# Optimization experiments

Hardware: AMD Instinct MI355X
Metric: run time of the kernel (lower is better)

The kernel has to match this reference:

```python
import jax, jax.numpy as jnp
import numpy as np

EPS = 1e-05
H, N, F = 1024, 16, 4096  # hidden_dim, state_dim, ffn_dim


def layernorm(x, g, b):
    mu = jnp.mean(x, axis=-1, keepdims=True)
    var = jnp.mean(jnp.square(x - mu), axis=-1, keepdims=True)
    return (x - mu) * jax.lax.rsqrt(var + EPS) * g + b


def setup_inputs() -> dict:
    key = jax.random.key(0)
    ks = jax.random.split(key, 12)
    B, L = 2, 2048
    s = lambda fan_in: 1.0 / np.sqrt(fan_in)
    inp = {
        "x": jax.random.normal(ks[0], (B, L, H), jnp.float32),
        "ln1_g": jnp.ones((H,), jnp.float32),
        "ln1_b": jnp.zeros((H,), jnp.float32),
        "Wd": jax.random.uniform(ks[1], (H, H), jnp.float32, -s(H), s(H)),
        "bd": jnp.zeros((H,), jnp.float32),
        "Wbc": jax.random.uniform(ks[2], (2 * N, H), jnp.float32, -s(H), s(H)),
        "bbc": jnp.zeros((2 * N,), jnp.float32),
        "A_log": jnp.log(jnp.tile(jnp.arange(1, N + 1, dtype=jnp.float32), (H, 1))),
        "D": jnp.ones((H,), jnp.float32),
        "ln2_g": jnp.ones((H,), jnp.float32),
        "ln2_b": jnp.zeros((H,), jnp.float32),
        "W1": jax.random.uniform(ks[3], (F, H), jnp.float32, -s(H), s(H)),
        "b1": jnp.zeros((F,), jnp.float32),
        "W2": jax.random.uniform(ks[4], (H, F), jnp.float32, -s(F), s(F)),
        "b2": jnp.zeros((H,), jnp.float32),
    }
    return inp


def _selective_ssm(xn, delta, Bm, Cm, A, D):
    # xn: (B,L,H)  delta: (B,L,H)  Bm,Cm: (B,L,N)  A: (H,N)  D: (H,)
    Bsz = xn.shape[0]
    # time-major for scan
    xs = (jnp.moveaxis(delta, 1, 0), jnp.moveaxis(Bm, 1, 0),
          jnp.moveaxis(Cm, 1, 0), jnp.moveaxis(xn, 1, 0))

    def step(h, t):
        d_t, b_t, c_t, x_t = t  # (B,H), (B,N), (B,N), (B,H)
        dA = jnp.exp(d_t[:, :, None] * A)                      # (B,H,N)
        dBx = d_t[:, :, None] * b_t[:, None, :] * x_t[:, :, None]
        h = dA * h + dBx                                       # (B,H,N)
        y = jnp.einsum('bhn,bn->bh', h, c_t)                   # (B,H)
        return h, y

    h0 = jnp.zeros((Bsz, H, N), xn.dtype)
    _, ys = jax.lax.scan(step, h0, xs)
    y = jnp.moveaxis(ys, 0, 1)  # (B,L,H)
    return y + D * xn


def reference(x, ln1_g, ln1_b, Wd, bd, Wbc, bbc, A_log, D,
              ln2_g, ln2_b, W1, b1, W2, b2):
    # --- SSMLayer: pre-norm selective SSM + residual ---
    xn = layernorm(x, ln1_g, ln1_b)
    delta = jax.nn.softplus(xn @ Wd.T + bd)      # (B,L,H)
    bc = xn @ Wbc.T + bbc                        # (B,L,2N)
    Bm, Cm = bc[..., :N], bc[..., N:]
    A = -jnp.exp(A_log)                          # (H,N), negative real
    ssm_out = x + _selective_ssm(xn, delta, Bm, Cm, A, D)
    # --- MambaBlock: norm -> FFN -> residual with ssm_out ---
    normed = layernorm(ssm_out, ln2_g, ln2_b)
    hff = jax.nn.gelu(normed @ W1.T + b1, approximate=False)
    ffn_out = hff @ W2.T + b2
    return ffn_out + ssm_out
```

## Files before the change

### kernel.cpp

```cpp
#include <hip/hip_runtime.h>
#include <cstdint>
#include <cstddef>

typedef unsigned short USHORT;
typedef __bf16 bf16x8 __attribute__((ext_vector_type(8)));
typedef float f32x4 __attribute__((ext_vector_type(4)));

__device__ __forceinline__ float b2f(USHORT u) {
    union { unsigned int i; float f; } v; v.i = ((unsigned int)u) << 16; return v.f;
}
__device__ __forceinline__ USHORT f2bf(float f) {
    union { float f; unsigned int i; } v; v.f = f;
    unsigned int u = v.i;
    unsigned int r = (u + 0x7FFFu + ((u >> 16) & 1u)) >> 16;
    return (USHORT)r;
}
__device__ __forceinline__ float fexp2(float x) { return __builtin_amdgcn_exp2f(x); }

__device__ __forceinline__ void gload_lds16(const void* g, void* l) {
    __builtin_amdgcn_global_load_lds(
        (const __attribute__((address_space(1))) void*)(uintptr_t)g,
        (__attribute__((address_space(3))) void*)(uint32_t)(uintptr_t)l,
        16, 0, 0);
}

__global__ __launch_bounds__(256)
void f2b_kernel(const float* __restrict__ src, USHORT* __restrict__ dst, int n)
{
    int i = (blockIdx.x * 256 + threadIdx.x) * 4;
    if (i < n) {
        float4 v = *(const float4*)(src + i);
        ushort4 o;
        o.x = f2bf(v.x); o.y = f2bf(v.y); o.z = f2bf(v.z); o.w = f2bf(v.w);
        *(ushort4*)(dst + i) = o;
    }
}

__global__ __launch_bounds__(256)
void ln_kernel(const float* __restrict__ inp, const float* __restrict__ g,
               const float* __restrict__ bsh, USHORT* __restrict__ out)
{
    const int tid = threadIdx.x;
    const size_t row = blockIdx.x;
    float4 t = ((const float4*)inp)[row * 256 + tid];
    float v[4] = { t.x, t.y, t.z, t.w };
    float s = v[0] + v[1] + v[2] + v[3];
    float sq = v[0]*v[0] + v[1]*v[1] + v[2]*v[2] + v[3]*v[3];
    #pragma unroll
    for (int off = 32; off; off >>= 1) { s += __shfl_down(s, off); sq += __shfl_down(sq, off); }
    __shared__ float red[8];
    const int wv = tid >> 6;
    if ((tid & 63) == 0) { red[wv] = s; red[wv + 4] = sq; }
    __syncthreads();
    const float S  = red[0] + red[1] + red[2] + red[3];
    const float SQ = red[4] + red[5] + red[6] + red[7];
    const float mu = S * (1.0f / 1024.0f);
    const float var = SQ * (1.0f / 1024.0f) - mu * mu;
    const float rs = rsqrtf(var + 1e-5f);
    float4 gv = ((const float4*)g)[tid];
    float4 bv = ((const float4*)bsh)[tid];
    ushort4 o;
    o.x = f2bf((v[0] - mu) * rs * gv.x + bv.x);
    o.y = f2bf((v[1] - mu) * rs * gv.y + bv.y);
    o.z = f2bf((v[2] - mu) * rs * gv.z + bv.z);
    o.w = f2bf((v[3] - mu) * rs * gv.w + bv.w);
    ((ushort4*)out)[row * 256 + tid] = o;
}

template<int EPI>
__global__ __launch_bounds__(256)
void gemm_bt(const USHORT* __restrict__ A, const USHORT* __restrict__ B,
             const float* __restrict__ bias, void* __restrict__ outp,
             void* __restrict__ outp2, int M, int N, int K, int lda, int ldb)
{
    __shared__ __align__(16) unsigned char smem[32768];
    USHORT* As = (USHORT*)smem;
    USHORT* Bs = (USHORT*)(smem + 8192);
    const int tid = threadIdx.x;
    const int lane = tid & 63;
    const int w = tid >> 6;
    const int wr = w >> 1, wc = w & 1;

    const int nx = gridDim.x, ny = gridDim.y;
    const int pid = blockIdx.y * nx + blockIdx.x;
    const int npg = 8 * nx;
    const int gid = pid / npg;
    const int first = gid * 8;
    const int rem = ny - first;
    const int gsz = (rem < 8) ? rem : 8;
    const int py = first + (pid % npg) % gsz;
    const int px = (pid % npg) / gsz;
    const int tm = py * 128;
    const int tn = px * 128;

    f32x4 acc[4][4];
    #pragma unroll
    for (int i = 0; i < 4; i++)
        #pragma unroll
        for (int j = 0; j < 4; j++) acc[i][j] = (f32x4){0.f, 0.f, 0.f, 0.f};

    const int srow = tid >> 2;
    const int scol = (tid & 3) * 8;
    const USHORT* gA0 = A + (size_t)(tm + srow) * lda + scol;
    const USHORT* gA1 = A + (size_t)(tm + 64 + srow) * lda + scol;
    const USHORT* gB0 = B + (size_t)(tn + srow) * ldb + scol;
    const USHORT* gB1 = B + (size_t)(tn + 64 + srow) * ldb + scol;
    USHORT* lA0 = As + w * 512;
    USHORT* lA1 = As + 2048 + w * 512;
    USHORT* lB0 = Bs + w * 512;
    USHORT* lB1 = Bs + 2048 + w * 512;

    const int fr = lane & 15;
    const int fko = (lane >> 4) * 8;
    const int quad = lane >> 4;

    for (int k0 = 0; k0 < K; k0 += 64) {
        gload_lds16(gA0 + k0, lA0);
        gload_lds16(gA1 + k0, lA1);
        gload_lds16(gB0 + k0, lB0);
        gload_lds16(gB1 + k0, lB1);
        gload_lds16(gA0 + k0 + 32, lA0 + 8192);
        gload_lds16(gA1 + k0 + 32, lA1 + 8192);
        gload_lds16(gB0 + k0 + 32, lB0 + 8192);
        gload_lds16(gB1 + k0 + 32, lB1 + 8192);
        __syncthreads();
        #pragma unroll
        for (int h = 0; h < 2; h++) {
            const USHORT* Ah = As + h * 8192;
            const USHORT* Bh = Bs + h * 8192;
            bf16x8 af[4], bfr[4];
            #pragma unroll
            for (int i = 0; i < 4; i++) {
                af[i]  = *(const bf16x8*)(Ah + (wr * 64 + i * 16 + fr) * 32 + fko);
                bfr[i] = *(const bf16x8*)(Bh + (wc * 64 + i * 16 + fr) * 32 + fko);
            }
            #pragma unroll
            for (int i = 0; i < 4; i++)
                #pragma unroll
                for (int j = 0; j < 4; j++)
                    acc[i][j] = __builtin_amdgcn_mfma_f32_16x16x32_bf16(af[i], bfr[j], acc[i][j], 0, 0, 0);
        }
        __syncthreads();
    }

    float* eW = (float*)(smem + (size_t)w * 4352);
    const int rr = lane >> 5;
    const int cc = lane & 31;
    const int gcolb = tn + wc * 64;
    float2 bvv = *(const float2*)&bias[gcolb + cc * 2];

    #pragma unroll
    for (int i = 0; i < 4; i++) {
        #pragma unroll
        for (int j = 0; j < 4; j++)
            #pragma unroll
            for (int r = 0; r < 4; r++)
                eW[(quad * 4 + r) * 68 + j * 16 + fr] = acc[i][j][r];
        __syncthreads();
        const int grow0 = tm + wr * 64 + i * 16;
        #pragma unroll
        for (int rp = 0; rp < 8; rp++) {
            const int row = rp * 2 + rr;
            const float2 v = *(const float2*)&eW[row * 68 + cc * 2];
            const size_t gidx = (size_t)(grow0 + row) * N + gcolb + cc * 2;
            if constexpr (EPI == 2) {
                const float z0 = v.x + bvv.x, z1 = v.y + bvv.y;
                const float o0 = (z0 > 20.f) ? z0 : 0.69314718f * __log2f(1.f + fexp2(z0 * 1.44269504f));
                const float o1 = (z1 > 20.f) ? z1 : 0.69314718f * __log2f(1.f + fexp2(z1 * 1.44269504f));
                *(float2*)((float*)outp + gidx) = make_float2(o0, o1);
            }
        }
        __syncthreads();
    }
    (void)outp2; (void)M;
}

template<int EPI>
__global__ __launch_bounds__(512)
void gemm256(const USHORT* __restrict__ A, const USHORT* __restrict__ B,
             const float* __restrict__ bias, void* __restrict__ outp,
             void* __restrict__ outp2, int M, int N, int K, int lda, int ldb)
{
    __shared__ __align__(16) unsigned char smem[131072];
    const int tid = threadIdx.x;
    const int lane = tid & 63;
    const int w = tid >> 6;
    const int wr = w >> 2;
    const int wc = w & 3;

    const int gx = gridDim.x;
    const int pid = blockIdx.y * gx + blockIdx.x;
    const int nwg = gx * gridDim.y;
    const int cpx = nwg >> 3;
    const int s = (pid & 7) * cpx + (pid >> 3);
    const int px = s % gx;
    const int py = s / gx;
    const int tm = py * 256;
    const int tn = px * 256;

    USHORT* po = nullptr;
    if constexpr (EPI == 3) {
        const int z = blockIdx.z;
        A += (size_t)z * K;
        B += (size_t)z * K;
        po = ((z < 2) ? (USHORT*)outp : (USHORT*)outp2) + (size_t)(z & 1) * ((size_t)M * N);
    }

    const int sr = tid >> 2;
    const int su = (tid & 3) ^ ((tid >> 3) & 3);
    const USHORT* gA0 = A + (size_t)(tm + sr) * lda + su * 8;
    const USHORT* gA1 = A + (size_t)(tm + 128 + sr) * lda + su * 8;
    const USHORT* gB0 = B + (size_t)(tn + sr) * ldb + su * 8;
    const USHORT* gB1 = B + (size_t)(tn + 128 + sr) * ldb + su * 8;

    const int fr = lane & 15;
    const int quad = lane >> 4;
    const int uR = quad ^ ((fr >> 1) & 3);
    const int loff = fr * 32 + uR * 8;

    f32x4 acc[8][4];
    #pragma unroll
    for (int i = 0; i < 8; i++)
        #pragma unroll
        for (int j = 0; j < 4; j++) acc[i][j] = (f32x4){0.f, 0.f, 0.f, 0.f};

    const int NT = K >> 5;

    auto stage = [&](int t) {
        unsigned char* sb = smem + (size_t)(t & 3) * 32768;
        const size_t koff = (size_t)t * 32;
        gload_lds16(gA0 + koff, sb + w * 1024);
        gload_lds16(gA1 + koff, sb + 8192 + w * 1024);
        gload_lds16(gB0 + koff, sb + 16384 + w * 1024);
        gload_lds16(gB1 + koff, sb + 24576 + w * 1024);
    };

    stage(0);
    stage(1);

    for (int t = 0; t < NT; ++t) {
        if (t + 1 < NT) asm volatile("s_waitcnt vmcnt(4)" ::: "memory");
        else            asm volatile("s_waitcnt vmcnt(0)" ::: "memory");
        __builtin_amdgcn_s_barrier();
        if (t + 2 < NT) stage(t + 2);

        const USHORT* sA = (const USHORT*)(smem + (size_t)(t & 3) * 32768);
        const USHORT* sB = sA + 8192;
        bf16x8 a[4], b[4];
        #pragma unroll
        for (int j = 0; j < 4; j++)
            b[j] = *(const bf16x8*)(sB + (wc * 64 + j * 16) * 32 + loff);
        #pragma unroll
        for (int i = 0; i < 4; i++)
            a[i] = *(const bf16x8*)(sA + (wr * 128 + i * 16) * 32 + loff);
        __builtin_amdgcn_s_setprio(1);
        #pragma unroll
        for (int i = 0; i < 4; i++)
            #pragma unroll
            for (int j = 0; j < 4; j++)
                acc[i][j] = __builtin_amdgcn_mfma_f32_16x16x32_bf16(a[i], b[j], acc[i][j], 0, 0, 0);
        __builtin_amdgcn_s_setprio(0);
        #pragma unroll
        for (int i = 0; i < 4; i++)
            a[i] = *(const bf16x8*)(sA + (wr * 128 + 64 + i * 16) * 32 + loff);
        __builtin_amdgcn_s_setprio(1);
        #pragma unroll
        for (int i = 0; i < 4; i++)
            #pragma unroll
            for (int j = 0; j < 4; j++)
                acc[4 + i][j] = __builtin_amdgcn_mfma_f32_16x16x32_bf16(a[i], b[j], acc[4 + i][j], 0, 0, 0);
        __builtin_amdgcn_s_setprio(0);
    }

    float* eW = (float*)(smem + (size_t)w * 4352);
    const int erow = lane >> 2;
    const int ecq = lane & 3;
    const int gcolb = tn + wc * 64 + ecq * 16;
    float bb[16];
    if constexpr (EPI == 1) {
        #pragma unroll
        for (int q = 0; q < 4; q++) {
            float4 bv = *(const float4*)&bias[gcolb + q * 4];
            bb[q*4+0] = bv.x; bb[q*4+1] = bv.y; bb[q*4+2] = bv.z; bb[q*4+3] = bv.w;
        }
    }
    #pragma unroll
    for (int i = 0; i < 8; i++) {
        #pragma unroll
        for (int j = 0; j < 4; j++)
            #pragma unroll
            for (int r = 0; r < 4; r++)
                eW[(quad * 4 + r) * 68 + j * 16 + fr] = acc[i][j][r];
        float v[16];
        #pragma unroll
        for (int q = 0; q < 4; q++) {
            float4 t4 = *(const float4*)&eW[erow * 68 + ecq * 16 + q * 4];
            v[q*4+0] = t4.x; v[q*4+1] = t4.y; v[q*4+2] = t4.z; v[q*4+3] = t4.w;
        }
        const int grow = tm + wr * 128 + i * 16 + erow;
        uint32_t pk[8];
        if constexpr (EPI == 1) {
            #pragma unroll
            for (int q = 0; q < 8; q++) {
                const float z0 = v[2*q]   + bb[2*q];
                const float z1 = v[2*q+1] + bb[2*q+1];
                const float u0 = z0 * (0.7978845608f + 0.035677408f * z0 * z0);
                const float u1 = z1 * (0.7978845608f + 0.035677408f * z1 * z1);
                const float s0 = __builtin_amdgcn_rcpf(1.f + fexp2(2.885390082f * u0));
                const float s1 = __builtin_amdgcn_rcpf(1.f + fexp2(2.885390082f * u1));
                const float g0 = z0 * (1.f - s0), g1 = z1 * (1.f - s1);
                pk[q] = (uint32_t)f2bf(g0) | ((uint32_t)f2bf(g1) << 16);
            }
            USHORT* op = (USHORT*)outp + (size_t)grow * N + gcolb;
            *(uint4*)op = make_uint4(pk[0], pk[1], pk[2], pk[3]);
            *(uint4*)(op + 8) = make_uint4(pk[4], pk[5], pk[6], pk[7]);
        } else {
            #pragma unroll
            for (int q = 0; q < 8; q++)
                pk[q] = (uint32_t)f2bf(v[2*q]) | ((uint32_t)f2bf(v[2*q+1]) << 16);
            USHORT* op = po + (size_t)grow * N + gcolb;
            *(uint4*)op = make_uint4(pk[0], pk[1], pk[2], pk[3]);
            *(uint4*)(op + 8) = make_uint4(pk[4], pk[5], pk[6], pk[7]);
        }
    }
}

__global__ __launch_bounds__(256)
void ffn2_reduce(const USHORT* __restrict__ p01, const USHORT* __restrict__ p23,
                 const float* __restrict__ bias, const float* __restrict__ extra,
                 float* __restrict__ out)
{
    const size_t PS = (size_t)4096 * 1024;
    const size_t i = ((size_t)blockIdx.x * 256 + threadIdx.x) * 4;
    ushort4 a = *(const ushort4*)(p01 + i);
    ushort4 b = *(const ushort4*)(p01 + PS + i);
    ushort4 c = *(const ushort4*)(p23 + i);
    ushort4 d = *(const ushort4*)(p23 + PS + i);
    float4 bv = *(const float4*)(bias + (i & 1023));
    float4 ev = *(const float4*)(extra + i);
    float4 o;
    o.x = b2f(a.x) + b2f(b.x) + b2f(c.x) + b2f(d.x) + bv.x + ev.x;
    o.y = b2f(a.y) + b2f(b.y) + b2f(c.y) + b2f(d.y) + bv.y + ev.y;
    o.z = b2f(a.z) + b2f(b.z) + b2f(c.z) + b2f(d.z) + bv.z + ev.z;
    o.w = b2f(a.w) + b2f(b.w) + b2f(c.w) + b2f(d.w) + bv.w + ev.w;
    *(float4*)(out + i) = o;
}

__global__ __launch_bounds__(256)
void bc_mfma(const USHORT* __restrict__ xn, const USHORT* __restrict__ WbcB,
             const float* __restrict__ bbc, float* __restrict__ bc)
{
    __shared__ __align__(16) USHORT As[64 * 32];
    __shared__ __align__(16) USHORT Bs[32 * 32];
    const int tid = threadIdx.x;
    const int lane = tid & 63;
    const int w = tid >> 6;
    const int tok0 = blockIdx.x * 64;

    const int srow = tid >> 2;
    const int scol = (tid & 3) * 8;
    const USHORT* gA = xn + (size_t)(tok0 + srow) * 1024 + scol;
    const USHORT* gB = WbcB + (size_t)srow * 1024 + scol;
    USHORT* lA = As + w * 512;
    USHORT* lB = Bs + w * 512;

    const int fr = lane & 15;
    const int fko = (lane >> 4) * 8;
    const int quad = lane >> 4;

    f32x4 acc[2];
    acc[0] = (f32x4){0.f, 0.f, 0.f, 0.f};
    acc[1] = (f32x4){0.f, 0.f, 0.f, 0.f};

    for (int k0 = 0; k0 < 1024; k0 += 32) {
        gload_lds16(gA + k0, lA);
        if (w < 2) gload_lds16(gB + k0, lB);
        __syncthreads();
        bf16x8 af = *(const bf16x8*)(As + (w * 16 + fr) * 32 + fko);
        bf16x8 b0 = *(const bf16x8*)(Bs + (fr) * 32 + fko);
        bf16x8 b1 = *(const bf16x8*)(Bs + (16 + fr) * 32 + fko);
        acc[0] = __builtin_amdgcn_mfma_f32_16x16x32_bf16(af, b0, acc[0], 0, 0, 0);
        acc[1] = __builtin_amdgcn_mfma_f32_16x16x32_bf16(af, b1, acc[1], 0, 0, 0);
        __syncthreads();
    }

    #pragma unroll
    for (int j = 0; j < 2; j++) {
        const int col = j * 16 + fr;
        const float bv = bbc[col];
        #pragma unroll
        for (int r = 0; r < 4; r++) {
            const int row = tok0 + w * 16 + quad * 4 + r;
            bc[(size_t)row * 32 + col] = acc[j][r] + bv;
        }
    }
}

#define SCAN_P 64
#define SCAN_T 32

__global__ __launch_bounds__(256)
void scan_pass1(const USHORT* __restrict__ xn, const float* __restrict__ delta,
                const float* __restrict__ bc, const float* __restrict__ Alog,
                float* __restrict__ sEnd, float* __restrict__ Ptot)
{
    const int tid = threadIdx.x;
    const int h = blockIdx.x * 256 + tid;
    const int b = blockIdx.y;
    const int p = blockIdx.z;
    const size_t tok0 = (size_t)b * 2048 + p * SCAN_T;

    __shared__ __align__(16) float sBC[SCAN_T][32];
    {
        int t = tid >> 3, q = (tid & 7) * 4;
        *(float4*)&sBC[t][q] = *(const float4*)(bc + (tok0 + t) * 32 + q);
    }

    float en[16], s[16], P[16];
    #pragma unroll
    for (int k = 0; k < 4; k++) {
        float4 a = *(const float4*)(Alog + h * 16 + k * 4);
        en[k*4+0] = -__expf(a.x) * 1.44269504f;
        en[k*4+1] = -__expf(a.y) * 1.44269504f;
        en[k*4+2] = -__expf(a.z) * 1.44269504f;
        en[k*4+3] = -__expf(a.w) * 1.44269504f;
    }
    #pragma unroll
    for (int n = 0; n < 16; n++) { s[n] = 0.f; P[n] = 1.f; }
    __syncthreads();

    const float* dp = delta + tok0 * 1024 + h;
    const USHORT* xp = xn + tok0 * 1024 + h;
    float d_c = dp[0];
    USHORT x_c = xp[0];
    for (int t = 0; t < SCAN_T; ++t) {
        const int tn = (t < SCAN_T - 1) ? t + 1 : t;
        float d_n = dp[(size_t)tn * 1024];
        USHORT x_n = xp[(size_t)tn * 1024];
        const float dx = d_c * b2f(x_c);
        #pragma unroll
        for (int k = 0; k < 4; k++) {
            float4 Bv = *(const float4*)&sBC[t][k*4];
            float bb[4] = { Bv.x, Bv.y, Bv.z, Bv.w };
            #pragma unroll
            for (int j = 0; j < 4; j++) {
                const int n = k*4 + j;
                const float dA = fexp2(d_c * en[n]);
                s[n] = fmaf(dA, s[n], dx * bb[j]);
                P[n] *= dA;
            }
        }
        d_c = d_n; x_c = x_n;
    }

    const size_t off = (size_t)p * 32768 + ((size_t)b * 1024 + h) * 16;
    #pragma unroll
    for (int k = 0; k < 4; k++) {
        *(float4*)(sEnd + off + k*4) = (float4){ s[k*4], s[k*4+1], s[k*4+2], s[k*4+3] };
        *(float4*)(Ptot + off + k*4) = (float4){ P[k*4], P[k*4+1], P[k*4+2], P[k*4+3] };
    }
}

__global__ __launch_bounds__(256)
void scan_mid(const float* __restrict__ sEnd, const float* __restrict__ Ptot,
              float* __restrict__ sIn)
{
    const int L = blockIdx.x * 256 + threadIdx.x;
    float s = 0.f;
    #pragma unroll 8
    for (int p = 0; p < SCAN_P; ++p) {
        const size_t off = (size_t)p * 32768 + L;
        sIn[off] = s;
        s = fmaf(Ptot[off], s, sEnd[off]);
    }
}

__global__ __launch_bounds__(256)
void scan_pass2(const float* __restrict__ x, const USHORT* __restrict__ xn,
                const float* __restrict__ delta, const float* __restrict__ bc,
                const float* __restrict__ Alog, const float* __restrict__ Dp,
                const float* __restrict__ sIn, float* __restrict__ ssm)
{
    const int tid = threadIdx.x;
    const int h = blockIdx.x * 256 + tid;
    const int b = blockIdx.y;
    const int p = blockIdx.z;
    const size_t tok0 = (size_t)b * 2048 + p * SCAN_T;

    __shared__ __align__(16) float sBC[SCAN_T][32];
    {
        int t = tid >> 3, q = (tid & 7) * 4;
        *(float4*)&sBC[t][q] = *(const float4*)(bc + (tok0 + t) * 32 + q);
    }

    float en[16], s[16];
    #pragma unroll
    for (int k = 0; k < 4; k++) {
        float4 a = *(const float4*)(Alog + h * 16 + k * 4);
        en[k*4+0] = -__expf(a.x) * 1.44269504f;
        en[k*4+1] = -__expf(a.y) * 1.44269504f;
        en[k*4+2] = -__expf(a.z) * 1.44269504f;
        en[k*4+3] = -__expf(a.w) * 1.44269504f;
    }
    const size_t off = (size_t)p * 32768 + ((size_t)b * 1024 + h) * 16;
    #pragma unroll
    for (int k = 0; k < 4; k++) {
        float4 v = *(const float4*)(sIn + off + k*4);
        s[k*4] = v.x; s[k*4+1] = v.y; s[k*4+2] = v.z; s[k*4+3] = v.w;
    }
    const float Dv = Dp[h];
    __syncthreads();

    const float* dp = delta + tok0 * 1024 + h;
    const USHORT* xp = xn + tok0 * 1024 + h;
    const float* xrp = x + tok0 * 1024 + h;
    float* op = ssm + tok0 * 1024 + h;

    float d_c = dp[0];
    USHORT x_c = xp[0];
    float xr_c = xrp[0];
    for (int t = 0; t < SCAN_T; ++t) {
        const int tn = (t < SCAN_T - 1) ? t + 1 : t;
        float d_n = dp[(size_t)tn * 1024];
        USHORT x_n = xp[(size_t)tn * 1024];
        float xr_n = xrp[(size_t)tn * 1024];
        const float xv = b2f(x_c);
        const float dx = d_c * xv;
        float y = 0.f;
        #pragma unroll
        for (int k = 0; k < 4; k++) {
            float4 Bv = *(const float4*)&sBC[t][k*4];
            float4 Cv = *(const float4*)&sBC[t][16 + k*4];
            float bb[4] = { Bv.x, Bv.y, Bv.z, Bv.w };
            float cc[4] = { Cv.x, Cv.y, Cv.z, Cv.w };
            #pragma unroll
            for (int j = 0; j < 4; j++) {
                const int n = k*4 + j;
                const float dA = fexp2(d_c * en[n]);
                s[n] = fmaf(dA, s[n], dx * bb[j]);
                y = fmaf(cc[j], s[n], y);
            }
        }
        op[(size_t)t * 1024] = xr_c + y + Dv * xv;
        d_c = d_n; x_c = x_n; xr_c = xr_n;
    }
}

extern "C" void kernel_launch(void* const* d_in, const int* in_sizes, int n_in,
                              void* d_out, int out_size, void* d_ws, size_t ws_size,
                              hipStream_t stream)
{
    const float* x    = (const float*)d_in[0];
    const float* ln1g = (const float*)d_in[1];
    const float* ln1b = (const float*)d_in[2];
    const float* Wd   = (const float*)d_in[3];
    const float* bd   = (const float*)d_in[4];
    const float* Wbc  = (const float*)d_in[5];
    const float* bbc  = (const float*)d_in[6];
    const float* Alog = (const float*)d_in[7];
    const float* Dp   = (const float*)d_in[8];
    const float* ln2g = (const float*)d_in[9];
    const float* ln2b = (const float*)d_in[10];
    const float* W1   = (const float*)d_in[11];
    const float* b1   = (const float*)d_in[12];
    const float* W2   = (const float*)d_in[13];
    const float* b2   = (const float*)d_in[14];
    float* out = (float*)d_out;

    char* ws = (char*)d_ws;
    const size_t MB = 1024 * 1024;
    float*  deltaW = (float*)(ws + 0);
    float*  ssmW   = (float*)(ws + 16 * MB);
    USHORT* xnW    = (USHORT*)(ws + 32 * MB);
    USHORT* nrmW   = (USHORT*)(ws + 40 * MB);
    USHORT* hffW   = (USHORT*)(ws + 48 * MB);
    float*  bcW    = (float*)(ws + 80 * MB);
    USHORT* WdB    = (USHORT*)(ws + 81 * MB);
    USHORT* W1B    = (USHORT*)(ws + 83 * MB);
    USHORT* W2B    = (USHORT*)(ws + 91 * MB);
    USHORT* WbcB   = (USHORT*)(ws + 99 * MB);
    float*  sEndW  = (float*)(ws + 48 * MB);
    float*  PtotW  = (float*)(ws + 56 * MB);
    float*  sInW   = (float*)(ws + 64 * MB);
    USHORT* ffn2p01 = (USHORT*)(ws + 0);
    USHORT* ffn2p23 = (USHORT*)(ws + 32 * MB);

    f2b_kernel<<<1024, 256, 0, stream>>>(Wd, WdB, 1024 * 1024);
    f2b_kernel<<<4096, 256, 0, stream>>>(W1, W1B, 4096 * 1024);
    f2b_kernel<<<4096, 256, 0, stream>>>(W2, W2B, 1024 * 4096);
    f2b_kernel<<<32, 256, 0, stream>>>(Wbc, WbcB, 32 * 1024);
    ln_kernel<<<4096, 256, 0, stream>>>(x, ln1g, ln1b, xnW);
    gemm_bt<2><<<dim3(8, 32), 256, 0, stream>>>(xnW, WdB, bd, deltaW, nullptr, 4096, 1024, 1024, 1024, 1024);
    bc_mfma<<<64, 256, 0, stream>>>(xnW, WbcB, bbc, bcW);
    scan_pass1<<<dim3(4, 2, SCAN_P), 256, 0, stream>>>(xnW, deltaW, bcW, Alog, sEndW, PtotW);
    scan_mid<<<128, 256, 0, stream>>>(sEndW, PtotW, sInW);
    scan_pass2<<<dim3(4, 2, SCAN_P), 256, 0, stream>>>(x, xnW, deltaW, bcW, Alog, Dp, sInW, ssmW);
    ln_kernel<<<4096, 256, 0, stream>>>(ssmW, ln2g, ln2b, nrmW);
    gemm256<1><<<dim3(16, 16), 512, 0, stream>>>(nrmW, W1B, b1, hffW, nullptr, 4096, 4096, 1024, 1024, 1024);
    gemm256<3><<<dim3(4, 16, 4), 512, 0, stream>>>(hffW, W2B, nullptr, ffn2p01, ffn2p23, 4096, 1024, 1024, 4096, 4096);
    ffn2_reduce<<<4096, 256, 0, stream>>>(ffn2p01, ffn2p23, b2, ssmW, out);

    (void)in_sizes; (void)n_in; (void)out_size; (void)ws_size;
}
```

Measured before the change: 306.3 us.

## Restructure 256x256 GEMM mainloop into K=64 double-buffered four-phase ping-pong schedule

The bf16 GEMM main loop moves from a 4-deep ring of K=32 stages to two 64KB buffers holding K=64 tiles, with a new 8-way XOR LDS swizzle for the 128-byte rows. Each iteration is split into four MFMA quadrants. Global-to-LDS loads for the next tile are spread between them, with barriers and partial vmcnt waits so memory traffic overlaps compute. The goal is fewer barriers per K element and better load/compute interleaving. In exchange it adds more barriers per iteration and tighter waitcnt bookkeeping that could stall or be subtly wrong.

```diff
diff --git a/kernel.cpp b/kernel.cpp
--- a/kernel.cpp
+++ b/kernel.cpp
@@ -192,9 +192,9 @@
     const int pid = blockIdx.y * gx + blockIdx.x;
     const int nwg = gx * gridDim.y;
     const int cpx = nwg >> 3;
-    const int s = (pid & 7) * cpx + (pid >> 3);
-    const int px = s % gx;
-    const int py = s / gx;
+    const int sw = (pid & 7) * cpx + (pid >> 3);
+    const int px = sw % gx;
+    const int py = sw / gx;
     const int tm = py * 256;
     const int tn = px * 256;
 
@@ -206,17 +206,18 @@
         po = ((z < 2) ? (USHORT*)outp : (USHORT*)outp2) + (size_t)(z & 1) * ((size_t)M * N);
     }
 
-    const int sr = tid >> 2;
-    const int su = (tid & 3) ^ ((tid >> 3) & 3);
-    const USHORT* gA0 = A + (size_t)(tm + sr) * lda + su * 8;
-    const USHORT* gA1 = A + (size_t)(tm + 128 + sr) * lda + su * 8;
-    const USHORT* gB0 = B + (size_t)(tn + sr) * ldb + su * 8;
-    const USHORT* gB1 = B + (size_t)(tn + 128 + sr) * ldb + su * 8;
+    const int srow = tid >> 3;
+    const int scol = ((tid & 7) ^ (srow & 7)) * 8;
+    const USHORT* gAs = A + (size_t)(tm + srow) * lda + scol;
+    const USHORT* gBs = B + (size_t)(tn + srow) * ldb + scol;
+    const size_t ldaH = (size_t)128 * lda;
+    const size_t ldbH = (size_t)128 * ldb;
+    const size_t ldaR = (size_t)64 * lda;
+    const size_t ldbR = (size_t)64 * ldb;
 
     const int fr = lane & 15;
     const int quad = lane >> 4;
-    const int uR = quad ^ ((fr >> 1) & 3);
-    const int loff = fr * 32 + uR * 8;
+    const int u0 = (quad ^ (fr & 7)) * 8;
 
     f32x4 acc[8][4];
     #pragma unroll
@@ -224,64 +225,137 @@
         #pragma unroll
         for (int j = 0; j < 4; j++) acc[i][j] = (f32x4){0.f, 0.f, 0.f, 0.f};
 
-    const int NT = K >> 5;
-
-    auto stage = [&](int t) {
-        unsigned char* sb = smem + (size_t)(t & 3) * 32768;
-        const size_t koff = (size_t)t * 32;
-        gload_lds16(gA0 + koff, sb + w * 1024);
-        gload_lds16(gA1 + koff, sb + 8192 + w * 1024);
-        gload_lds16(gB0 + koff, sb + 16384 + w * 1024);
-        gload_lds16(gB1 + koff, sb + 24576 + w * 1024);
-    };
-
-    stage(0);
-    stage(1);
+    const int NT = K >> 6;
+
+    {
+        unsigned char* b0 = smem;
+        gload_lds16(gAs,               b0 +     0 + w * 1024);
+        gload_lds16(gAs + ldaR,        b0 +  8192 + w * 1024);
+        gload_lds16(gBs,               b0 + 32768 + w * 1024);
+        gload_lds16(gBs + ldbR,        b0 + 40960 + w * 1024);
+        gload_lds16(gAs + ldaH,        b0 + 16384 + w * 1024);
+        gload_lds16(gAs + ldaH + ldaR, b0 + 24576 + w * 1024);
+        gload_lds16(gBs + ldbH,        b0 + 49152 + w * 1024);
+        gload_lds16(gBs + ldbH + ldbR, b0 + 57344 + w * 1024);
+    }
+    asm volatile("s_waitcnt vmcnt(4)" ::: "memory");
+    __builtin_amdgcn_s_barrier();
+
+    bf16x8 aL[4][2], aH[4][2], bb[2][2];
 
     for (int t = 0; t < NT; ++t) {
-        if (t + 1 < NT) asm volatile("s_waitcnt vmcnt(4)" ::: "memory");
-        else            asm volatile("s_waitcnt vmcnt(0)" ::: "memory");
-        __builtin_amdgcn_s_barrier();
-        if (t + 2 < NT) stage(t + 2);
-
-        const USHORT* sA = (const USHORT*)(smem + (size_t)(t & 3) * 32768);
-        const USHORT* sB = sA + 8192;
-        bf16x8 a[4], b[4];
-        #pragma unroll
-        for (int j = 0; j < 4; j++)
-            b[j] = *(const bf16x8*)(sB + (wc * 64 + j * 16) * 32 + loff);
-        #pragma unroll
-        for (int i = 0; i < 4; i++)
-            a[i] = *(const bf16x8*)(sA + (wr * 128 + i * 16) * 32 + loff);
+        const bool nl = (t + 1 < NT);
+        const USHORT* base = (const USHORT*)(smem + (size_t)(t & 1) * 65536);
+        const USHORT* sAh = base + wr * 8192;
+        const USHORT* sBh = base + 16384 + (wc >> 1) * 8192;
+        const int brow0 = (wc & 1) * 64;
+        unsigned char* nb = smem + (size_t)((t + 1) & 1) * 65536;
+        const size_t kn = (size_t)(t + 1) * 64;
+
+        #pragma unroll
+        for (int ii = 0; ii < 4; ii++) {
+            const USHORT* rp = sAh + (ii * 16 + fr) * 64;
+            aL[ii][0] = *(const bf16x8*)(rp + u0);
+            aL[ii][1] = *(const bf16x8*)(rp + (u0 ^ 32));
+        }
+        #pragma unroll
+        for (int jj = 0; jj < 2; jj++) {
+            const USHORT* rp = sBh + (brow0 + jj * 16 + fr) * 64;
+            bb[jj][0] = *(const bf16x8*)(rp + u0);
+            bb[jj][1] = *(const bf16x8*)(rp + (u0 ^ 32));
+        }
+        if (nl) {
+            gload_lds16(gAs + kn,        nb +    0 + w * 1024);
+            gload_lds16(gAs + kn + ldaR, nb + 8192 + w * 1024);
+        }
+        __builtin_amdgcn_s_barrier();
         __builtin_amdgcn_s_setprio(1);
         #pragma unroll
-        for (int i = 0; i < 4; i++)
-            #pragma unroll
-            for (int j = 0; j < 4; j++)
-                acc[i][j] = __builtin_amdgcn_mfma_f32_16x16x32_bf16(a[i], b[j], acc[i][j], 0, 0, 0);
+        for (int ii = 0; ii < 4; ii++)
+            #pragma unroll
+            for (int jj = 0; jj < 2; jj++) {
+                acc[ii][jj] = __builtin_amdgcn_mfma_f32_16x16x32_bf16(aL[ii][0], bb[jj][0], acc[ii][jj], 0, 0, 0);
+                acc[ii][jj] = __builtin_amdgcn_mfma_f32_16x16x32_bf16(aL[ii][1], bb[jj][1], acc[ii][jj], 0, 0, 0);
+            }
         __builtin_amdgcn_s_setprio(0);
-        #pragma unroll
-        for (int i = 0; i < 4; i++)
-            a[i] = *(const bf16x8*)(sA + (wr * 128 + 64 + i * 16) * 32 + loff);
+        if (nl) asm volatile("s_waitcnt vmcnt(4)" ::: "memory");
+        else    asm volatile("s_waitcnt vmcnt(2)" ::: "memory");
+        __builtin_amdgcn_s_barrier();
+
+        #pragma unroll
+        for (int ii = 0; ii < 4; ii++) {
+            const USHORT* rp = sAh + (64 + ii * 16 + fr) * 64;
+            aH[ii][0] = *(const bf16x8*)(rp + u0);
+            aH[ii][1] = *(const bf16x8*)(rp + (u0 ^ 32));
+        }
+        if (nl) {
+            gload_lds16(gBs + kn,        nb + 32768 + w * 1024);
+            gload_lds16(gBs + kn + ldbR, nb + 40960 + w * 1024);
+        }
+        __builtin_amdgcn_s_barrier();
         __builtin_amdgcn_s_setprio(1);
         #pragma unroll
-        for (int i = 0; i < 4; i++)
-            #pragma unroll
-            for (int j = 0; j < 4; j++)
-                acc[4 + i][j] = __builtin_amdgcn_mfma_f32_16x16x32_bf16(a[i], b[j], acc[4 + i][j], 0, 0, 0);
+        for (int ii = 0; ii < 4; ii++)
+            #pragma unroll
+            for (int jj = 0; jj < 2; jj++) {
+                acc[4 + ii][jj] = __builtin_amdgcn_mfma_f32_16x16x32_bf16(aH[ii][0], bb[jj][0], acc[4 + ii][jj], 0, 0, 0);
+                acc[4 + ii][jj] = __builtin_amdgcn_mfma_f32_16x16x32_bf16(aH[ii][1], bb[jj][1], acc[4 + ii][jj], 0, 0, 0);
+            }
         __builtin_amdgcn_s_setprio(0);
+        if (nl) asm volatile("s_waitcnt vmcnt(4)" ::: "memory");
+        else    asm volatile("s_waitcnt vmcnt(0)" ::: "memory");
+        __builtin_amdgcn_s_barrier();
+
+        #pragma unroll
+        for (int jj = 0; jj < 2; jj++) {
+            const USHORT* rp = sBh + (brow0 + 32 + jj * 16 + fr) * 64;
+            bb[jj][0] = *(const bf16x8*)(rp + u0);
+            bb[jj][1] = *(const bf16x8*)(rp + (u0 ^ 32));
+        }
+        if (nl) {
+            gload_lds16(gAs + ldaH + kn,        nb + 16384 + w * 1024);
+            gload_lds16(gAs + ldaH + kn + ldaR, nb + 24576 + w * 1024);
+        }
+        __builtin_amdgcn_s_barrier();
+        __builtin_amdgcn_s_setprio(1);
+        #pragma unroll
+        for (int ii = 0; ii < 4; ii++)
+            #pragma unroll
+            for (int jj = 0; jj < 2; jj++) {
+                acc[4 + ii][2 + jj] = __builtin_amdgcn_mfma_f32_16x16x32_bf16(aH[ii][0], bb[jj][0], acc[4 + ii][2 + jj], 0, 0, 0);
+                acc[4 + ii][2 + jj] = __builtin_amdgcn_mfma_f32_16x16x32_bf16(aH[ii][1], bb[jj][1], acc[4 + ii][2 + jj], 0, 0, 0);
+            }
+        __builtin_amdgcn_s_setprio(0);
+        __builtin_amdgcn_s_barrier();
+
+        if (nl) {
+            gload_lds16(gBs + ldbH + kn,        nb + 49152 + w * 1024);
+            gload_lds16(gBs + ldbH + kn + ldbR, nb + 57344 + w * 1024);
+        }
+        __builtin_amdgcn_s_barrier();
+        __builtin_amdgcn_s_setprio(1);
+        #pragma unroll
+        for (int ii = 0; ii < 4; ii++)
+            #pragma unroll
+            for (int jj = 0; jj < 2; jj++) {
+                acc[ii][2 + jj] = __builtin_amdgcn_mfma_f32_16x16x32_bf16(aL[ii][0], bb[jj][0], acc[ii][2 + jj], 0, 0, 0);
+                acc[ii][2 + jj] = __builtin_amdgcn_mfma_f32_16x16x32_bf16(aL[ii][1], bb[jj][1], acc[ii][2 + jj], 0, 0, 0);
+            }
+        __builtin_amdgcn_s_setprio(0);
+        if (nl) asm volatile("s_waitcnt vmcnt(4)" ::: "memory");
+        __builtin_amdgcn_s_barrier();
     }
 
     float* eW = (float*)(smem + (size_t)w * 4352);
     const int erow = lane >> 2;
     const int ecq = lane & 3;
     const int gcolb = tn + wc * 64 + ecq * 16;
-    float bb[16];
+    float bbv[16];
     if constexpr (EPI == 1) {
         #pragma unroll
         for (int q = 0; q < 4; q++) {
             float4 bv = *(const float4*)&bias[gcolb + q * 4];
-            bb[q*4+0] = bv.x; bb[q*4+1] = bv.y; bb[q*4+2] = bv.z; bb[q*4+3] = bv.w;
+            bbv[q*4+0] = bv.x; bbv[q*4+1] = bv.y; bbv[q*4+2] = bv.z; bbv[q*4+3] = bv.w;
         }
     }
     #pragma unroll
@@ -302,12 +376,12 @@
         if constexpr (EPI == 1) {
             #pragma unroll
             for (int q = 0; q < 8; q++) {
-                const float z0 = v[2*q]   + bb[2*q];
-                const float z1 = v[2*q+1] + bb[2*q+1];
-                const float u0 = z0 * (0.7978845608f + 0.035677408f * z0 * z0);
-                const float u1 = z1 * (0.7978845608f + 0.035677408f * z1 * z1);
-                const float s0 = __builtin_amdgcn_rcpf(1.f + fexp2(2.885390082f * u0));
-                const float s1 = __builtin_amdgcn_rcpf(1.f + fexp2(2.885390082f * u1));
+                const float z0 = v[2*q]   + bbv[2*q];
+                const float z1 = v[2*q+1] + bbv[2*q+1];
+                const float u0g = z0 * (0.7978845608f + 0.035677408f * z0 * z0);
+                const float u1g = z1 * (0.7978845608f + 0.035677408f * z1 * z1);
+                const float s0 = __builtin_amdgcn_rcpf(1.f + fexp2(2.885390082f * u0g));
+                const float s1 = __builtin_amdgcn_rcpf(1.f + fexp2(2.885390082f * u1g));
                 const float g0 = z0 * (1.f - s0), g1 = z1 * (1.f - s1);
                 pk[q] = (uint32_t)f2bf(g0) | ((uint32_t)f2bf(g1) << 16);
             }
```

Result: no change. 305.2 us (-0.3%).

## Add 128x256-tile triple-buffered GEMM for split-K FFN2 with swizzled block order

Applied to the files above, without the earlier changes.

Adds a new GEMM kernel with 128x256 output tiles, K-step 32, three LDS stages and direct global-to-LDS loads. It also uses a grouped block-index swizzle and raises MFMA priority while issuing. The FFN2 split-K GEMM now uses it, launching 512 workgroups instead of 256 to improve occupancy and overlap of loads with compute. The cost is a smaller K-step per barrier, which adds synchronisation overhead, plus duplicated epilogue code.

```diff
diff --git a/kernel.cpp b/kernel.cpp
--- a/kernel.cpp
+++ b/kernel.cpp
@@ -325,6 +325,145 @@
     }
 }
 
+template<int EPI>
+__global__ __launch_bounds__(512)
+void gemm_tlp(const USHORT* __restrict__ A, const USHORT* __restrict__ B,
+              const float* __restrict__ bias, void* __restrict__ outp,
+              void* __restrict__ outp2, int M, int N, int K, int lda, int ldb)
+{
+    __shared__ __align__(16) unsigned char smem[73728];
+    const int tid = threadIdx.x;
+    const int lane = tid & 63;
+    const int w = tid >> 6;
+    const int wr = w >> 2;
+    const int wc = w & 3;
+
+    const int gx = gridDim.x;
+    const int pid = blockIdx.y * gx + blockIdx.x;
+    const int nwg = gx * gridDim.y;
+    const int cpx = nwg >> 3;
+    const int sw = (pid & 7) * cpx + (pid >> 3);
+    const int tm = (sw % gx) * 128;
+    const int tn = (sw / gx) * 256;
+
+    USHORT* po = nullptr;
+    if constexpr (EPI == 3) {
+        const int z = blockIdx.z;
+        A += (size_t)z * K;
+        B += (size_t)z * K;
+        po = ((z < 2) ? (USHORT*)outp : (USHORT*)outp2) + (size_t)(z & 1) * ((size_t)M * N);
+    }
+
+    const int srow = tid >> 2;
+    const int su = (tid & 3) ^ ((tid >> 3) & 3);
+    const USHORT* gA  = A + (size_t)(tm + srow) * lda + su * 8;
+    const USHORT* gB0 = B + (size_t)(tn + srow) * ldb + su * 8;
+    const USHORT* gB1 = B + (size_t)(tn + 128 + srow) * ldb + su * 8;
+
+    const int fr = lane & 15;
+    const int quad = lane >> 4;
+    const int uR = quad ^ ((fr >> 1) & 3);
+    const int loff = fr * 32 + uR * 8;
+
+    f32x4 acc[4][4];
+    #pragma unroll
+    for (int i = 0; i < 4; i++)
+        #pragma unroll
+        for (int j = 0; j < 4; j++) acc[i][j] = (f32x4){0.f, 0.f, 0.f, 0.f};
+
+    const int NT = K >> 5;
+
+    auto stage = [&](int t) {
+        unsigned char* sb = smem + (size_t)(t % 3) * 24576;
+        const size_t ko = (size_t)t * 32;
+        gload_lds16(gA  + ko, sb +         w * 1024);
+        gload_lds16(gB0 + ko, sb +  8192 + w * 1024);
+        gload_lds16(gB1 + ko, sb + 16384 + w * 1024);
+    };
+
+    stage(0);
+    stage(1);
+
+    for (int t = 0; t < NT; ++t) {
+        if (t + 2 < NT) { stage(t + 2); asm volatile("s_waitcnt vmcnt(6)" ::: "memory"); }
+        else if (t + 1 < NT) asm volatile("s_waitcnt vmcnt(3)" ::: "memory");
+        else                 asm volatile("s_waitcnt vmcnt(0)" ::: "memory");
+        __builtin_amdgcn_s_barrier();
+
+        const USHORT* sA = (const USHORT*)(smem + (size_t)(t % 3) * 24576);
+        const USHORT* sB = sA + 4096;
+        bf16x8 a[4], b[4];
+        #pragma unroll
+        for (int j = 0; j < 4; j++)
+            b[j] = *(const bf16x8*)(sB + (wc * 64 + j * 16) * 32 + loff);
+        #pragma unroll
+        for (int i = 0; i < 4; i++)
+            a[i] = *(const bf16x8*)(sA + (wr * 64 + i * 16) * 32 + loff);
+        __builtin_amdgcn_s_setprio(1);
+        #pragma unroll
+        for (int i = 0; i < 4; i++)
+            #pragma unroll
+            for (int j = 0; j < 4; j++)
+                acc[i][j] = __builtin_amdgcn_mfma_f32_16x16x32_bf16(a[i], b[j], acc[i][j], 0, 0, 0);
+        __builtin_amdgcn_s_setprio(0);
+        __builtin_amdgcn_s_barrier();
+    }
+
+    __syncthreads();
+    float* eW = (float*)(smem + (size_t)w * 4352);
+    const int erow = lane >> 2;
+    const int ecq = lane & 3;
+    const int gcolb = tn + wc * 64 + ecq * 16;
+    float bb[16];
+    if constexpr (EPI == 1) {
+        #pragma unroll
+        for (int q = 0; q < 4; q++) {
+            float4 bv = *(const float4*)&bias[gcolb + q * 4];
+            bb[q*4+0] = bv.x; bb[q*4+1] = bv.y; bb[q*4+2] = bv.z; bb[q*4+3] = bv.w;
+        }
+    }
+    #pragma unroll
+    for (int i = 0; i < 4; i++) {
+        #pragma unroll
+        for (int j = 0; j < 4; j++)
+            #pragma unroll
+            for (int r = 0; r < 4; r++)
+                eW[(quad * 4 + r) * 68 + j * 16 + fr] = acc[i][j][r];
+        float v[16];
+        #pragma unroll
+        for (int q = 0; q < 4; q++) {
+            float4 t4 = *(const float4*)&eW[erow * 68 + ecq * 16 + q * 4];
+            v[q*4+0] = t4.x; v[q*4+1] = t4.y; v[q*4+2] = t4.z; v[q*4+3] = t4.w;
+        }
+        const int grow = tm + wr * 64 + i * 16 + erow;
+        uint32_t pk[8];
+        if constexpr (EPI == 1) {
+            #pragma unroll
+            for (int q = 0; q < 8; q++) {
+                const float z0 = v[2*q]   + bb[2*q];
+                const float z1 = v[2*q+1] + bb[2*q+1];
+                const float u0 = z0 * (0.7978845608f + 0.035677408f * z0 * z0);
+                const float u1 = z1 * (0.7978845608f + 0.035677408f * z1 * z1);
+                const float s0 = __builtin_amdgcn_rcpf(1.f + fexp2(2.885390082f * u0));
+                const float s1 = __builtin_amdgcn_rcpf(1.f + fexp2(2.885390082f * u1));
+                const float g0 = z0 * (1.f - s0), g1 = z1 * (1.f - s1);
+                pk[q] = (uint32_t)f2bf(g0) | ((uint32_t)f2bf(g1) << 16);
+            }
+            USHORT* op = (USHORT*)outp + (size_t)grow * N + gcolb;
+            *(uint4*)op = make_uint4(pk[0], pk[1], pk[2], pk[3]);
+            *(uint4*)(op + 8) = make_uint4(pk[4], pk[5], pk[6], pk[7]);
+        } else {
+            #pragma unroll
+            for (int q = 0; q < 8; q++)
+                pk[q] = (uint32_t)f2bf(v[2*q]) | ((uint32_t)f2bf(v[2*q+1]) << 16);
+            USHORT* op = po + (size_t)grow * N + gcolb;
+            *(uint4*)op = make_uint4(pk[0], pk[1], pk[2], pk[3]);
+            *(uint4*)(op + 8) = make_uint4(pk[4], pk[5], pk[6], pk[7]);
+        }
+    }
+    (void)bias;
+}
+
 __global__ __launch_bounds__(256)
 void ffn2_reduce(const USHORT* __restrict__ p01, const USHORT* __restrict__ p23,
                  const float* __restrict__ bias, const float* __restrict__ extra,
@@ -597,7 +736,7 @@
     scan_pass2<<<dim3(4, 2, SCAN_P), 256, 0, stream>>>(x, xnW, deltaW, bcW, Alog, Dp, sInW, ssmW);
     ln_kernel<<<4096, 256, 0, stream>>>(ssmW, ln2g, ln2b, nrmW);
     gemm256<1><<<dim3(16, 16), 512, 0, stream>>>(nrmW, W1B, b1, hffW, nullptr, 4096, 4096, 1024, 1024, 1024);
-    gemm256<3><<<dim3(4, 16, 4), 512, 0, stream>>>(hffW, W2B, nullptr, ffn2p01, ffn2p23, 4096, 1024, 1024, 4096, 4096);
+    gemm_tlp<3><<<dim3(32, 4, 4), 512, 0, stream>>>(hffW, W2B, nullptr, ffn2p01, ffn2p23, 4096, 1024, 1024, 4096, 4096);
     ffn2_reduce<<<4096, 256, 0, stream>>>(ffn2p01, ffn2p23, b2, ssmW, out);
 
     (void)in_sizes; (void)n_in; (void)out_size; (void)ws_size;
```

Measured after the change: 315.3 us. 1.03x slower.
